# Optimization experiments

Measured on AMD Instinct MI355X. Metric: run time of the kernel, lower is better.

The kernel has to match this reference:

```python
import jax, jax.numpy as jnp
import numpy as np

N_EMBD = 1024
D_K = 1024
D_V = 1024

def setup_inputs() -> dict:
    key = jax.random.key(0)
    k1, k2, k3, k4 = jax.random.split(key, 4)
    B, T = 4, 2048
    std = N_EMBD ** -0.5
    x = jax.random.normal(k1, (B, T, N_EMBD), dtype=jnp.float32)
    Wq = jax.random.normal(k2, (N_EMBD, D_K), dtype=jnp.float32) * std
    Wk = jax.random.normal(k3, (N_EMBD, D_K), dtype=jnp.float32) * std
    Wv = jax.random.normal(k4, (N_EMBD, D_V), dtype=jnp.float32) * std
    return {"x": x, "Wq": Wq, "Wk": Wk, "Wv": Wv}

def reference(x, Wq, Wk, Wv):
    # x: [B, T, C]
    T = x.shape[1]
    q = x @ Wq  # [B, T, d_k]
    k = x @ Wk  # [B, T, d_k]
    v = x @ Wv  # [B, T, d_v]
    scale = Wk.shape[1] ** -0.5
    wei = jnp.einsum('btd,bsd->bts', q, k) * scale  # [B, T, T]
    causal = jnp.tril(jnp.ones((T, T), dtype=bool))
    wei = jnp.where(causal, wei, -jnp.inf)
    wei = jax.nn.softmax(wei, axis=-1)
    return wei @ v  # [B, T, d_v]
```

## Files before the change

kernel.cpp:

```cpp
#include <hip/hip_runtime.h>
#include <hip/hip_bf16.h>
#include <stdint.h>

using bf16_t = __hip_bfloat16;
typedef __bf16 bf16x8 __attribute__((ext_vector_type(8)));
typedef float f32x4 __attribute__((ext_vector_type(4)));

__device__ __forceinline__ void async_lds16(const void* g, void* l) {
  __builtin_amdgcn_global_load_lds(
      (const __attribute__((address_space(1))) void*)g,
      (__attribute__((address_space(3))) void*)l, 16, 0, 0);
}

__device__ __forceinline__ unsigned short f2bf_u16(float f) {
  __hip_bfloat16 h = __float2bfloat16(f);
  return __builtin_bit_cast(unsigned short, h);
}

__device__ __forceinline__ float bf2f(unsigned short u) {
  __hip_bfloat16 h = __builtin_bit_cast(__hip_bfloat16, u);
  return __bfloat162float(h);
}

__global__ __launch_bounds__(256) void convert_all_kernel(
    const float* __restrict__ x, bf16_t* __restrict__ xb,
    const float* __restrict__ Wq, const float* __restrict__ Wk,
    const float* __restrict__ Wv, bf16_t* __restrict__ wt) {
  __shared__ bf16_t tile[32][33];
  const int bid = blockIdx.x;
  if (bid < 8192) {
    size_t i = ((size_t)bid * 256 + threadIdx.x) * 4;
    float4 v = *(const float4*)(x + i);
    ushort4 o;
    o.x = f2bf_u16(v.x);
    o.y = f2bf_u16(v.y);
    o.z = f2bf_u16(v.z);
    o.w = f2bf_u16(v.w);
    *(ushort4*)(xb + i) = o;
    return;
  }
  const int w = bid - 8192;
  const int z = w >> 10;
  const int bxy = w & 1023;
  const float* W = (z == 0) ? Wq : (z == 1) ? Wk : Wv;
  bf16_t* WT = wt + (size_t)z * 1024 * 1024;
  const int tx = threadIdx.x & 31;
  const int ty = threadIdx.x >> 5;
  const int bx = bxy & 31;
  const int by = bxy >> 5;
  const int k0 = by * 32, n0 = bx * 32;
#pragma unroll
  for (int j = 0; j < 32; j += 8)
    tile[ty + j][tx] = __float2bfloat16(W[(size_t)(k0 + ty + j) * 1024 + n0 + tx]);
  __syncthreads();
#pragma unroll
  for (int j = 0; j < 32; j += 8)
    WT[(size_t)(n0 + ty + j) * 1024 + k0 + tx] = tile[tx][ty + j];
}

template <int OUT_MODE, bool CAUSAL_SKIP, bool KLIMIT, bool XCDSWZ>
__global__ __launch_bounds__(512, 2) void gemm_pipe_kernel(
    const bf16_t* __restrict__ A, const bf16_t* __restrict__ BT,
    void* __restrict__ Cv, void* __restrict__ Cv2, void* __restrict__ Cv3,
    int M, int N, int K, int lda, int ldb, int ldc,
    long long aBatch, long long bBatch, long long cBatch) {
  int bx = blockIdx.x, by = blockIdx.y;
  if (XCDSWZ) {
    const int gx = gridDim.x;
    const int nwg = gx * gridDim.y;
    const int id = by * gx + bx;
    const int cpx = nwg >> 3;
    const int swz = (id & 7) * cpx + (id >> 3);
    by = swz / gx;
    bx = swz % gx;
  }
  const int m0 = by * 128;
  const int n0 = bx * 256;
  if (CAUSAL_SKIP && 2 * bx > by) return;
  A += (size_t)blockIdx.z * aBatch;
  BT += (size_t)blockIdx.z * bBatch;
  int nkt = K >> 5;
  if (KLIMIT) {
    int lim = (m0 + 128) >> 5;
    nkt = nkt < lim ? nkt : lim;
  }

  __shared__ bf16_t lsA[3 * 128 * 32];
  __shared__ bf16_t lsB[3 * 256 * 32];

  const int tid = threadIdx.x;
  const int wid = tid >> 6;
  const int lane = tid & 63;
  const int wm = wid >> 2;
  const int wn = wid & 3;

  const int sr = tid >> 2;
  const int ss = tid & 3;
  const int sswz = ss ^ ((sr >> 1) & 3);
  const bf16_t* gA = A + (size_t)(m0 + sr) * lda + sswz * 8;
  const bf16_t* gB0 = BT + (size_t)(n0 + sr) * ldb + sswz * 8;
  const bf16_t* gB1 = BT + (size_t)(n0 + 128 + sr) * ldb + sswz * 8;

  const int kslot = (lane >> 4) ^ ((lane >> 1) & 3);
  const int abase = (wm * 64 + (lane & 15)) * 32 + kslot * 8;
  const int bbase = (wn * 64 + (lane & 15)) * 32 + kslot * 8;

  f32x4 acc[4][4];
  const f32x4 zero = {0.f, 0.f, 0.f, 0.f};
#pragma unroll
  for (int m = 0; m < 4; ++m)
#pragma unroll
    for (int n = 0; n < 4; ++n) acc[m][n] = zero;

  async_lds16(gA, lsA + wid * 512);
  async_lds16(gB0, lsB + wid * 512);
  async_lds16(gB1, lsB + 4096 + wid * 512);
  if (nkt > 1) {
    async_lds16(gA + 32, lsA + 4096 + wid * 512);
    async_lds16(gB0 + 32, lsB + 8192 + wid * 512);
    async_lds16(gB1 + 32, lsB + 8192 + 4096 + wid * 512);
    asm volatile("s_waitcnt vmcnt(3)" ::: "memory");
  } else {
    asm volatile("s_waitcnt vmcnt(0)" ::: "memory");
  }
  __builtin_amdgcn_s_barrier();

  int cb = 0;
  for (int t = 0; t < nkt; ++t) {
    const bf16_t* bufA = lsA + cb * 4096;
    const bf16_t* bufB = lsB + cb * 8192;
    int sb = cb + 2;
    if (sb >= 3) sb -= 3;

    bf16x8 af[4], bfr[4];
#pragma unroll
    for (int mf = 0; mf < 4; ++mf)
      af[mf] = *(const bf16x8*)(bufA + abase + mf * 512);
    bfr[0] = *(const bf16x8*)(bufB + bbase);
    bfr[1] = *(const bf16x8*)(bufB + bbase + 512);
    if (t + 2 < nkt) {
      async_lds16(gA + (t + 2) * 32, lsA + sb * 4096 + wid * 512);
      async_lds16(gB0 + (t + 2) * 32, lsB + sb * 8192 + wid * 512);
    }
    __builtin_amdgcn_s_barrier();
    __builtin_amdgcn_s_setprio(1);
#pragma unroll
    for (int mf = 0; mf < 4; ++mf)
#pragma unroll
      for (int nf = 0; nf < 2; ++nf)
        acc[mf][nf] = __builtin_amdgcn_mfma_f32_16x16x32_bf16(
            af[mf], bfr[nf], acc[mf][nf], 0, 0, 0);
    __builtin_amdgcn_s_setprio(0);
    __builtin_amdgcn_s_barrier();

    bfr[2] = *(const bf16x8*)(bufB + bbase + 1024);
    bfr[3] = *(const bf16x8*)(bufB + bbase + 1536);
    if (t + 2 < nkt)
      async_lds16(gB1 + (t + 2) * 32, lsB + sb * 8192 + 4096 + wid * 512);
    if (t + 2 < nkt) {
      asm volatile("s_waitcnt vmcnt(3)" ::: "memory");
    } else if (t + 2 == nkt) {
      asm volatile("s_waitcnt vmcnt(0)" ::: "memory");
    }
    __builtin_amdgcn_s_barrier();
    __builtin_amdgcn_s_setprio(1);
#pragma unroll
    for (int mf = 0; mf < 4; ++mf)
#pragma unroll
      for (int nf = 2; nf < 4; ++nf)
        acc[mf][nf] = __builtin_amdgcn_mfma_f32_16x16x32_bf16(
            af[mf], bfr[nf], acc[mf][nf], 0, 0, 0);
    __builtin_amdgcn_s_setprio(0);
    __builtin_amdgcn_s_barrier();

    cb = cb + 1;
    if (cb >= 3) cb -= 3;
  }

  const int erow = wm * 64 + (lane >> 4) * 4;
  const int ecol = wn * 64 + (lane & 15);
  if (OUT_MODE == 2) {
    float* C = (float*)Cv + (size_t)blockIdx.z * cBatch;
#pragma unroll
    for (int m = 0; m < 4; ++m)
#pragma unroll
      for (int n = 0; n < 4; ++n)
#pragma unroll
        for (int j = 0; j < 4; ++j) {
          int r = m0 + erow + m * 16 + j;
          int c = n0 + ecol + n * 16;
          C[(size_t)r * ldc + c] = acc[m][n][j];
        }
  } else if (OUT_MODE == 4) {
    bf16_t* C = (bf16_t*)Cv + (size_t)blockIdx.z * cBatch;
#pragma unroll
    for (int m = 0; m < 4; ++m)
#pragma unroll
      for (int n = 0; n < 4; ++n)
#pragma unroll
        for (int j = 0; j < 4; ++j) {
          int r = m0 + erow + m * 16 + j;
          int c = n0 + ecol + n * 16;
          C[(size_t)r * ldc + c] = __float2bfloat16(acc[m][n][j]);
        }
  } else {
    if (n0 < 2048) {
      bf16_t* C = (bf16_t*)((n0 < 1024) ? Cv : Cv2);
      const int cb0 = n0 & 1023;
#pragma unroll
      for (int m = 0; m < 4; ++m)
#pragma unroll
        for (int n = 0; n < 4; ++n)
#pragma unroll
          for (int j = 0; j < 4; ++j) {
            int r = m0 + erow + m * 16 + j;
            int c = cb0 + ecol + n * 16;
            C[(size_t)r * 1024 + c] = __float2bfloat16(acc[m][n][j]);
          }
    } else {
      bf16_t* C = (bf16_t*)Cv3;
      const int d0 = n0 - 2048;
#pragma unroll
      for (int m = 0; m < 4; ++m)
#pragma unroll
        for (int n = 0; n < 4; ++n)
#pragma unroll
          for (int j = 0; j < 4; ++j) {
            int r = m0 + erow + m * 16 + j;
            int d = d0 + ecol + n * 16;
            int b = r >> 11, tt = r & 2047;
            C[((size_t)b * 1024 + d) * 2048 + tt] = __float2bfloat16(acc[m][n][j]);
          }
    }
  }
}

__global__ __launch_bounds__(256) void softmax_causal_kernel(bf16_t* __restrict__ Sb) {
  const int lane = threadIdx.x & 63;
  const int rg = blockIdx.x * 4 + (threadIdx.x >> 6);
  const int b = rg >> 11;
  const int t = rg & 2047;
  bf16_t* srow = Sb + (size_t)b * 8388608 + (size_t)t * 4096;
  const int qmax = t >> 8;

  float v[8][4];
#pragma unroll
  for (int it = 0; it < 8; ++it) {
    if (it <= qmax) {
      ushort4 u = *(const ushort4*)(srow + (it * 64 + lane) * 4);
      v[it][0] = bf2f(u.x);
      v[it][1] = bf2f(u.y);
      v[it][2] = bf2f(u.z);
      v[it][3] = bf2f(u.w);
    } else {
      v[it][0] = v[it][1] = v[it][2] = v[it][3] = 0.f;
    }
  }

  float mx = -3.0e38f;
#pragma unroll
  for (int it = 0; it < 8; ++it) {
    int s0 = (it * 64 + lane) * 4;
    if (s0 + 0 <= t) mx = fmaxf(mx, v[it][0]);
    if (s0 + 1 <= t) mx = fmaxf(mx, v[it][1]);
    if (s0 + 2 <= t) mx = fmaxf(mx, v[it][2]);
    if (s0 + 3 <= t) mx = fmaxf(mx, v[it][3]);
  }
#pragma unroll
  for (int off = 32; off > 0; off >>= 1) mx = fmaxf(mx, __shfl_xor(mx, off, 64));

  const float kMul = 0.03125f * 1.4426950408889634f;
  float p[8][4];
  float sum = 0.f;
#pragma unroll
  for (int it = 0; it < 8; ++it) {
    int s0 = (it * 64 + lane) * 4;
    float e0 = (s0 + 0 <= t) ? exp2f((v[it][0] - mx) * kMul) : 0.f;
    float e1 = (s0 + 1 <= t) ? exp2f((v[it][1] - mx) * kMul) : 0.f;
    float e2 = (s0 + 2 <= t) ? exp2f((v[it][2] - mx) * kMul) : 0.f;
    float e3 = (s0 + 3 <= t) ? exp2f((v[it][3] - mx) * kMul) : 0.f;
    p[it][0] = e0; p[it][1] = e1; p[it][2] = e2; p[it][3] = e3;
    sum += (e0 + e1) + (e2 + e3);
  }
#pragma unroll
  for (int off = 32; off > 0; off >>= 1) sum += __shfl_xor(sum, off, 64);
  const float inv = 1.f / sum;

#pragma unroll
  for (int it = 0; it < 8; ++it) {
    if (it <= qmax) {
      ushort4 o;
      o.x = f2bf_u16(p[it][0] * inv);
      o.y = f2bf_u16(p[it][1] * inv);
      o.z = f2bf_u16(p[it][2] * inv);
      o.w = f2bf_u16(p[it][3] * inv);
      *(ushort4*)(srow + (it * 64 + lane) * 4) = o;
    }
  }
}

extern "C" void kernel_launch(void* const* d_in, const int* in_sizes, int n_in,
                              void* d_out, int out_size, void* d_ws, size_t ws_size,
                              hipStream_t stream) {
  (void)in_sizes; (void)n_in; (void)out_size;
  const float* x = (const float*)d_in[0];
  const float* Wq = (const float*)d_in[1];
  const float* Wk = (const float*)d_in[2];
  const float* Wv = (const float*)d_in[3];
  float* out = (float*)d_out;

  char* ws = (char*)d_ws;
  const size_t NEED = 123731968;
  const bool batched = ws_size >= NEED;

  bf16_t* xb = (bf16_t*)ws;
  bf16_t* Sb;
  bf16_t *WT, *Qb, *Kb, *VT;
  if (batched) {
    Sb = (bf16_t*)ws;
    WT = (bf16_t*)(ws + 67108864);
    Qb = (bf16_t*)(ws + 73400320);
    Kb = (bf16_t*)(ws + 90177536);
    VT = (bf16_t*)(ws + 106954752);
  } else {
    Sb = (bf16_t*)ws;
    WT = (bf16_t*)(ws + 16777216);
    Qb = (bf16_t*)(ws + 16777216 + 6291456);
    Kb = Qb + 8388608;
    VT = Kb + 8388608;
  }

  convert_all_kernel<<<11264, 256, 0, stream>>>(x, xb, Wq, Wk, Wv, WT);

  gemm_pipe_kernel<3, false, false, true><<<dim3(12, 64, 1), 512, 0, stream>>>(
      xb, WT, Qb, Kb, VT, 8192, 3072, 1024, 1024, 1024, 0, 0, 0, 0);

  if (batched) {
    gemm_pipe_kernel<4, true, false, false><<<dim3(8, 16, 4), 512, 0, stream>>>(
        Qb, Kb, Sb, nullptr, nullptr, 2048, 2048, 1024, 1024, 1024, 4096,
        2097152LL, 2097152LL, 8388608LL);
    softmax_causal_kernel<<<2048, 256, 0, stream>>>(Sb);
    gemm_pipe_kernel<2, false, true, false><<<dim3(4, 16, 4), 512, 0, stream>>>(
        Sb, VT, out, nullptr, nullptr, 2048, 1024, 2048, 4096,
        2048, 1024, 8388608LL, 2097152LL, 2097152LL);
  } else {
    for (int b = 0; b < 4; ++b) {
      const size_t qoff = (size_t)b * 2048 * 1024;
      gemm_pipe_kernel<4, true, false, false><<<dim3(8, 16, 1), 512, 0, stream>>>(
          Qb + qoff, Kb + qoff, Sb, nullptr, nullptr, 2048, 2048, 1024, 1024,
          1024, 4096, 0, 0, 0);
      softmax_causal_kernel<<<512, 256, 0, stream>>>(Sb);
      gemm_pipe_kernel<2, false, true, false><<<dim3(4, 16, 1), 512, 0, stream>>>(
          Sb, VT + qoff, out + qoff, nullptr, nullptr, 2048,
          1024, 2048, 4096, 2048, 1024, 0, 0, 0);
    }
  }
}
```

Baseline: 179.9 us.

## Add 256x256-tile GEMM with 64-wide K steps for QKV projection

After: 186.0 us. 3.4% more time.

```diff
diff --git a/kernel.cpp b/kernel.cpp
--- a/kernel.cpp
+++ b/kernel.cpp
@@ -58,12 +58,11 @@
     WT[(size_t)(n0 + ty + j) * 1024 + k0 + tx] = tile[tx][ty + j];
 }
 
-template <int OUT_MODE, bool CAUSAL_SKIP, bool KLIMIT, bool XCDSWZ>
-__global__ __launch_bounds__(512, 2) void gemm_pipe_kernel(
+template <int OUT_MODE, bool XCDSWZ>
+__global__ __launch_bounds__(512, 2) void gemm256_kernel(
     const bf16_t* __restrict__ A, const bf16_t* __restrict__ BT,
     void* __restrict__ Cv, void* __restrict__ Cv2, void* __restrict__ Cv3,
-    int M, int N, int K, int lda, int ldb, int ldc,
-    long long aBatch, long long bBatch, long long cBatch) {
+    int M, int N, int K, int lda, int ldb, int ldc) {
   int bx = blockIdx.x, by = blockIdx.y;
   if (XCDSWZ) {
     const int gx = gridDim.x;
@@ -74,6 +73,182 @@
     by = swz / gx;
     bx = swz % gx;
   }
+  const int m0 = by * 256;
+  const int n0 = bx * 256;
+  const int nkt = K >> 6;
+
+  __shared__ bf16_t lsA[2 * 16384];
+  __shared__ bf16_t lsB[2 * 16384];
+
+  const int tid = threadIdx.x;
+  const int wid = tid >> 6;
+  const int lane = tid & 63;
+  const int wm = wid >> 2;
+  const int wn = wid & 3;
+
+  const int sr = tid >> 2;
+  const int sswz = (tid & 3) ^ ((tid >> 3) & 3);
+  const bf16_t* gA0 = A + (size_t)(m0 + sr) * lda + sswz * 8;
+  const bf16_t* gA1 = A + (size_t)(m0 + 128 + sr) * lda + sswz * 8;
+  const bf16_t* gB0 = BT + (size_t)(n0 + sr) * ldb + sswz * 8;
+  const bf16_t* gB1 = BT + (size_t)(n0 + 128 + sr) * ldb + sswz * 8;
+
+  auto stageA = [&](int t, int kh) {
+    bf16_t* d = lsA + ((t & 1) << 14) + (kh << 13) + (wid << 9);
+    const size_t co = (size_t)(t << 6) + (kh << 5);
+    async_lds16(gA0 + co, d);
+    async_lds16(gA1 + co, d + 4096);
+  };
+  auto stageB = [&](int t, int kh) {
+    bf16_t* d = lsB + ((t & 1) << 14) + (kh << 13) + (wid << 9);
+    const size_t co = (size_t)(t << 6) + (kh << 5);
+    async_lds16(gB0 + co, d);
+    async_lds16(gB1 + co, d + 4096);
+  };
+
+  const int kswz = ((lane >> 4) ^ ((lane >> 1) & 3)) * 8;
+  const int aRd = (wm * 128 + (lane & 15)) * 32 + kswz;
+  const int bRd = (wn * 64 + (lane & 15)) * 32 + kswz;
+
+  f32x4 acc[8][4];
+  const f32x4 zero = {0.f, 0.f, 0.f, 0.f};
+#pragma unroll
+  for (int m = 0; m < 8; ++m)
+#pragma unroll
+    for (int n = 0; n < 4; ++n) acc[m][n] = zero;
+
+  stageA(0, 0);
+  stageB(0, 0);
+  stageA(0, 1);
+  stageB(0, 1);
+  if (nkt > 1) {
+    stageA(1, 0);
+    stageB(1, 0);
+    asm volatile("s_waitcnt vmcnt(4)" ::: "memory");
+  } else {
+    asm volatile("s_waitcnt vmcnt(0)" ::: "memory");
+  }
+  __builtin_amdgcn_s_barrier();
+
+  bf16x8 af[4], bfr[4];
+
+#define PHASE_TAIL()                                      \
+  __builtin_amdgcn_s_barrier();                           \
+  asm volatile("s_waitcnt lgkmcnt(0)" ::: "memory");      \
+  __builtin_amdgcn_s_setprio(1);
+
+#define MFMA16(mh)                                        \
+  _Pragma("unroll") for (int mf = 0; mf < 4; ++mf)        \
+      _Pragma("unroll") for (int nf = 0; nf < 4; ++nf)    \
+          acc[(mh)*4 + mf][nf] = __builtin_amdgcn_mfma_f32_16x16x32_bf16( \
+              af[mf], bfr[nf], acc[(mh)*4 + mf][nf], 0, 0, 0);
+
+  for (int t = 0; t < nkt; ++t) {
+    const bf16_t* bufA = lsA + ((t & 1) << 14);
+    const bf16_t* bufB = lsB + ((t & 1) << 14);
+
+#pragma unroll
+    for (int nf = 0; nf < 4; ++nf)
+      bfr[nf] = *(const bf16x8*)(bufB + (nf << 9) + bRd);
+#pragma unroll
+    for (int mf = 0; mf < 4; ++mf)
+      af[mf] = *(const bf16x8*)(bufA + (mf << 9) + aRd);
+    if (t + 1 < nkt) stageA(t + 1, 1);
+    PHASE_TAIL()
+    MFMA16(0)
+    __builtin_amdgcn_s_setprio(0);
+    __builtin_amdgcn_s_barrier();
+
+#pragma unroll
+    for (int mf = 0; mf < 4; ++mf)
+      af[mf] = *(const bf16x8*)(bufA + ((mf + 4) << 9) + aRd);
+    if (t + 1 < nkt) stageB(t + 1, 1);
+    PHASE_TAIL()
+    MFMA16(1)
+    __builtin_amdgcn_s_setprio(0);
+    __builtin_amdgcn_s_barrier();
+
+#pragma unroll
+    for (int nf = 0; nf < 4; ++nf)
+      bfr[nf] = *(const bf16x8*)(bufB + 8192 + (nf << 9) + bRd);
+#pragma unroll
+    for (int mf = 0; mf < 4; ++mf)
+      af[mf] = *(const bf16x8*)(bufA + 8192 + (mf << 9) + aRd);
+    if (t + 2 < nkt) stageA(t + 2, 0);
+    PHASE_TAIL()
+    MFMA16(0)
+    __builtin_amdgcn_s_setprio(0);
+    __builtin_amdgcn_s_barrier();
+
+#pragma unroll
+    for (int mf = 0; mf < 4; ++mf)
+      af[mf] = *(const bf16x8*)(bufA + 8192 + ((mf + 4) << 9) + aRd);
+    if (t + 2 < nkt) stageB(t + 2, 0);
+    PHASE_TAIL()
+    MFMA16(1)
+    __builtin_amdgcn_s_setprio(0);
+    if (t + 2 < nkt) {
+      asm volatile("s_waitcnt vmcnt(4)" ::: "memory");
+    } else if (t + 1 < nkt) {
+      asm volatile("s_waitcnt vmcnt(0)" ::: "memory");
+    }
+    __builtin_amdgcn_s_barrier();
+  }
+#undef PHASE_TAIL
+#undef MFMA16
+
+  const int erow = wm * 128 + (lane >> 4) * 4;
+  const int ecol = wn * 64 + (lane & 15);
+  if (OUT_MODE == 2) {
+    float* C = (float*)Cv;
+#pragma unroll
+    for (int m = 0; m < 8; ++m)
+#pragma unroll
+      for (int n = 0; n < 4; ++n)
+#pragma unroll
+        for (int j = 0; j < 4; ++j) {
+          int r = m0 + erow + m * 16 + j;
+          int c = n0 + ecol + n * 16;
+          C[(size_t)r * ldc + c] = acc[m][n][j];
+        }
+  } else {
+    if (n0 < 2048) {
+      bf16_t* C = (bf16_t*)((n0 < 1024) ? Cv : Cv2);
+      const int cb0 = n0 & 1023;
+#pragma unroll
+      for (int m = 0; m < 8; ++m)
+#pragma unroll
+        for (int n = 0; n < 4; ++n)
+#pragma unroll
+          for (int j = 0; j < 4; ++j) {
+            int r = m0 + erow + m * 16 + j;
+            int c = cb0 + ecol + n * 16;
+            C[(size_t)r * 1024 + c] = __float2bfloat16(acc[m][n][j]);
+          }
+    } else {
+      bf16_t* C = (bf16_t*)Cv3;
+      const int d0 = n0 - 2048;
+#pragma unroll
+      for (int m = 0; m < 8; ++m)
+#pragma unroll
+        for (int n = 0; n < 4; ++n)
+#pragma unroll
+          for (int j = 0; j < 4; ++j) {
+            int r = m0 + erow + m * 16 + j;
+            int d = d0 + ecol + n * 16;
+            int b = r >> 11, tt = r & 2047;
+            C[((size_t)b * 1024 + d) * 2048 + tt] = __float2bfloat16(acc[m][n][j]);
+          }
+    }
+  }
+}
+
+template <int OUT_MODE, bool CAUSAL_SKIP, bool KLIMIT>
+__global__ __launch_bounds__(512, 2) void gemm_pipe_kernel(
+    const bf16_t* __restrict__ A, const bf16_t* __restrict__ BT,
+    void* __restrict__ Cv, int M, int N, int K, int lda, int ldb, int ldc,
+    long long aBatch, long long bBatch, long long cBatch) {
+  const int bx = blockIdx.x, by = blockIdx.y;
   const int m0 = by * 128;
   const int n0 = bx * 256;
   if (CAUSAL_SKIP && 2 * bx > by) return;
@@ -191,7 +366,7 @@
           int c = n0 + ecol + n * 16;
           C[(size_t)r * ldc + c] = acc[m][n][j];
         }
-  } else if (OUT_MODE == 4) {
+  } else {
     bf16_t* C = (bf16_t*)Cv + (size_t)blockIdx.z * cBatch;
 #pragma unroll
     for (int m = 0; m < 4; ++m)
@@ -203,35 +378,6 @@
           int c = n0 + ecol + n * 16;
           C[(size_t)r * ldc + c] = __float2bfloat16(acc[m][n][j]);
         }
-  } else {
-    if (n0 < 2048) {
-      bf16_t* C = (bf16_t*)((n0 < 1024) ? Cv : Cv2);
-      const int cb0 = n0 & 1023;
-#pragma unroll
-      for (int m = 0; m < 4; ++m)
-#pragma unroll
-        for (int n = 0; n < 4; ++n)
-#pragma unroll
-          for (int j = 0; j < 4; ++j) {
-            int r = m0 + erow + m * 16 + j;
-            int c = cb0 + ecol + n * 16;
-            C[(size_t)r * 1024 + c] = __float2bfloat16(acc[m][n][j]);
-          }
-    } else {
-      bf16_t* C = (bf16_t*)Cv3;
-      const int d0 = n0 - 2048;
-#pragma unroll
-      for (int m = 0; m < 4; ++m)
-#pragma unroll
-        for (int n = 0; n < 4; ++n)
-#pragma unroll
-          for (int j = 0; j < 4; ++j) {
-            int r = m0 + erow + m * 16 + j;
-            int d = d0 + ecol + n * 16;
-            int b = r >> 11, tt = r & 2047;
-            C[((size_t)b * 1024 + d) * 2048 + tt] = __float2bfloat16(acc[m][n][j]);
-          }
-    }
   }
 }
 
@@ -332,27 +478,27 @@
 
   convert_all_kernel<<<11264, 256, 0, stream>>>(x, xb, Wq, Wk, Wv, WT);
 
-  gemm_pipe_kernel<3, false, false, true><<<dim3(12, 64, 1), 512, 0, stream>>>(
-      xb, WT, Qb, Kb, VT, 8192, 3072, 1024, 1024, 1024, 0, 0, 0, 0);
+  gemm256_kernel<3, true><<<dim3(12, 32, 1), 512, 0, stream>>>(
+      xb, WT, Qb, Kb, VT, 8192, 3072, 1024, 1024, 1024, 0);
 
   if (batched) {
-    gemm_pipe_kernel<4, true, false, false><<<dim3(8, 16, 4), 512, 0, stream>>>(
-        Qb, Kb, Sb, nullptr, nullptr, 2048, 2048, 1024, 1024, 1024, 4096,
+    gemm_pipe_kernel<4, true, false><<<dim3(8, 16, 4), 512, 0, stream>>>(
+        Qb, Kb, Sb, 2048, 2048, 1024, 1024, 1024, 4096,
         2097152LL, 2097152LL, 8388608LL);
     softmax_causal_kernel<<<2048, 256, 0, stream>>>(Sb);
-    gemm_pipe_kernel<2, false, true, false><<<dim3(4, 16, 4), 512, 0, stream>>>(
-        Sb, VT, out, nullptr, nullptr, 2048, 1024, 2048, 4096,
-        2048, 1024, 8388608LL, 2097152LL, 2097152LL);
+    gemm_pipe_kernel<2, false, true><<<dim3(4, 16, 4), 512, 0, stream>>>(
+        Sb, VT, out, 2048, 1024, 2048, 4096, 2048, 1024,
+        8388608LL, 2097152LL, 2097152LL);
   } else {
     for (int b = 0; b < 4; ++b) {
       const size_t qoff = (size_t)b * 2048 * 1024;
-      gemm_pipe_kernel<4, true, false, false><<<dim3(8, 16, 1), 512, 0, stream>>>(
-          Qb + qoff, Kb + qoff, Sb, nullptr, nullptr, 2048, 2048, 1024, 1024,
-          1024, 4096, 0, 0, 0);
+      gemm_pipe_kernel<4, true, false><<<dim3(8, 16, 1), 512, 0, stream>>>(
+          Qb + qoff, Kb + qoff, Sb, 2048, 2048, 1024, 1024, 1024, 4096,
+          0, 0, 0);
       softmax_causal_kernel<<<512, 256, 0, stream>>>(Sb);
-      gemm_pipe_kernel<2, false, true, false><<<dim3(4, 16, 1), 512, 0, stream>>>(
-          Sb, VT + qoff, out + qoff, nullptr, nullptr, 2048,
-          1024, 2048, 4096, 2048, 1024, 0, 0, 0);
-    }
-  }
-}
+      gemm_pipe_kernel<2, false, true><<<dim3(4, 16, 1), 512, 0, stream>>>(
+          Sb, VT + qoff, out + qoff, 2048, 1024, 2048, 4096, 2048, 1024,
+          0, 0, 0);
+    }
+  }
+}
```

## Use 128x128 tiles for attention GEMMs with paired causal row balancing

Applied to the files above, without the earlier changes.

Result: faster. 174.8 us (-2.9%).

```diff
diff --git a/kernel.cpp b/kernel.cpp
--- a/kernel.cpp
+++ b/kernel.cpp
@@ -58,14 +58,13 @@
     WT[(size_t)(n0 + ty + j) * 1024 + k0 + tx] = tile[tx][ty + j];
 }
 
-template <int OUT_MODE, bool CAUSAL_SKIP, bool KLIMIT, bool XCDSWZ>
+template <int OUT_MODE>
 __global__ __launch_bounds__(512, 2) void gemm_pipe_kernel(
     const bf16_t* __restrict__ A, const bf16_t* __restrict__ BT,
     void* __restrict__ Cv, void* __restrict__ Cv2, void* __restrict__ Cv3,
-    int M, int N, int K, int lda, int ldb, int ldc,
-    long long aBatch, long long bBatch, long long cBatch) {
+    int M, int N, int K, int lda, int ldb) {
   int bx = blockIdx.x, by = blockIdx.y;
-  if (XCDSWZ) {
+  {
     const int gx = gridDim.x;
     const int nwg = gx * gridDim.y;
     const int id = by * gx + bx;
@@ -76,14 +75,7 @@
   }
   const int m0 = by * 128;
   const int n0 = bx * 256;
-  if (CAUSAL_SKIP && 2 * bx > by) return;
-  A += (size_t)blockIdx.z * aBatch;
-  BT += (size_t)blockIdx.z * bBatch;
-  int nkt = K >> 5;
-  if (KLIMIT) {
-    int lim = (m0 + 128) >> 5;
-    nkt = nkt < lim ? nkt : lim;
-  }
+  const int nkt = K >> 5;
 
   __shared__ bf16_t lsA[3 * 128 * 32];
   __shared__ bf16_t lsB[3 * 256 * 32];
@@ -179,8 +171,9 @@
 
   const int erow = wm * 64 + (lane >> 4) * 4;
   const int ecol = wn * 64 + (lane & 15);
-  if (OUT_MODE == 2) {
-    float* C = (float*)Cv + (size_t)blockIdx.z * cBatch;
+  if (n0 < 2048) {
+    bf16_t* C = (bf16_t*)((n0 < 1024) ? Cv : Cv2);
+    const int cb0 = n0 & 1023;
 #pragma unroll
     for (int m = 0; m < 4; ++m)
 #pragma unroll
@@ -188,11 +181,12 @@
 #pragma unroll
         for (int j = 0; j < 4; ++j) {
           int r = m0 + erow + m * 16 + j;
-          int c = n0 + ecol + n * 16;
-          C[(size_t)r * ldc + c] = acc[m][n][j];
+          int c = cb0 + ecol + n * 16;
+          C[(size_t)r * 1024 + c] = __float2bfloat16(acc[m][n][j]);
         }
-  } else if (OUT_MODE == 4) {
-    bf16_t* C = (bf16_t*)Cv + (size_t)blockIdx.z * cBatch;
+  } else {
+    bf16_t* C = (bf16_t*)Cv3;
+    const int d0 = n0 - 2048;
 #pragma unroll
     for (int m = 0; m < 4; ++m)
 #pragma unroll
@@ -200,36 +194,130 @@
 #pragma unroll
         for (int j = 0; j < 4; ++j) {
           int r = m0 + erow + m * 16 + j;
-          int c = n0 + ecol + n * 16;
-          C[(size_t)r * ldc + c] = __float2bfloat16(acc[m][n][j]);
+          int d = d0 + ecol + n * 16;
+          int b = r >> 11, tt = r & 2047;
+          C[((size_t)b * 1024 + d) * 2048 + tt] = __float2bfloat16(acc[m][n][j]);
         }
-  } else {
-    if (n0 < 2048) {
-      bf16_t* C = (bf16_t*)((n0 < 1024) ? Cv : Cv2);
-      const int cb0 = n0 & 1023;
+  }
+}
+
+template <int OUT_MODE, bool CAUSAL_SKIP, bool PAIRED>
+__global__ __launch_bounds__(512, 2) void gemm128_kernel(
+    const bf16_t* __restrict__ A, const bf16_t* __restrict__ BT,
+    void* __restrict__ Cv, int K, int lda, int ldb, int ldc,
+    long long aBatch, long long bBatch, long long cBatch) {
+  const int bx = blockIdx.x, by = blockIdx.y;
+  if (CAUSAL_SKIP && bx > by) return;
+  const bf16_t* Ab = A + (size_t)blockIdx.z * aBatch;
+  const bf16_t* Bb = BT + (size_t)blockIdx.z * bBatch;
+
+  __shared__ bf16_t lsA[3 * 4096];
+  __shared__ bf16_t lsB[3 * 4096];
+
+  const int tid = threadIdx.x;
+  const int wid = tid >> 6;
+  const int lane = tid & 63;
+  const int wm = wid >> 2;
+  const int wn = wid & 3;
+
+  const int sr = tid >> 2;
+  const int sswz = (tid & 3) ^ ((sr >> 1) & 3);
+  const int n0 = bx * 128;
+  const bf16_t* gB = Bb + (size_t)(n0 + sr) * ldb + sswz * 8;
+
+  const int kslot = (lane >> 4) ^ ((lane >> 1) & 3);
+  const int aRd = (wm * 64 + (lane & 15)) * 32 + kslot * 8;
+  const int bRd = (wn * 32 + (lane & 15)) * 32 + kslot * 8;
+
+  const int njobs = PAIRED ? 2 : 1;
+  for (int job = 0; job < njobs; ++job) {
+    const int byE = (PAIRED && job) ? (15 - by) : by;
+    const int m0 = byE * 128;
+    int nkt = K >> 5;
+    if (PAIRED) {
+      int lim = (m0 + 128) >> 5;
+      nkt = nkt < lim ? nkt : lim;
+    }
+    const bf16_t* gA = Ab + (size_t)(m0 + sr) * lda + sswz * 8;
+
+    f32x4 acc[4][2];
+    const f32x4 zero = {0.f, 0.f, 0.f, 0.f};
+#pragma unroll
+    for (int m = 0; m < 4; ++m)
+#pragma unroll
+      for (int n = 0; n < 2; ++n) acc[m][n] = zero;
+
+    async_lds16(gA, lsA + wid * 512);
+    async_lds16(gB, lsB + wid * 512);
+    if (nkt > 1) {
+      async_lds16(gA + 32, lsA + 4096 + wid * 512);
+      async_lds16(gB + 32, lsB + 4096 + wid * 512);
+      asm volatile("s_waitcnt vmcnt(2)" ::: "memory");
+    } else {
+      asm volatile("s_waitcnt vmcnt(0)" ::: "memory");
+    }
+    __builtin_amdgcn_s_barrier();
+
+    int cb = 0;
+    for (int t = 0; t < nkt; ++t) {
+      const bf16_t* bufA = lsA + cb * 4096;
+      const bf16_t* bufB = lsB + cb * 4096;
+      int sb = cb + 2;
+      if (sb >= 3) sb -= 3;
+
+      bf16x8 af[4], bfr[2];
+#pragma unroll
+      for (int mf = 0; mf < 4; ++mf)
+        af[mf] = *(const bf16x8*)(bufA + aRd + mf * 512);
+      bfr[0] = *(const bf16x8*)(bufB + bRd);
+      bfr[1] = *(const bf16x8*)(bufB + bRd + 512);
+      if (t + 2 < nkt) {
+        async_lds16(gA + (t + 2) * 32, lsA + sb * 4096 + wid * 512);
+        async_lds16(gB + (t + 2) * 32, lsB + sb * 4096 + wid * 512);
+        asm volatile("s_waitcnt vmcnt(2)" ::: "memory");
+      } else if (t + 2 == nkt) {
+        asm volatile("s_waitcnt vmcnt(0)" ::: "memory");
+      }
+      __builtin_amdgcn_s_barrier();
+      __builtin_amdgcn_s_setprio(1);
+#pragma unroll
+      for (int mf = 0; mf < 4; ++mf)
+#pragma unroll
+        for (int nf = 0; nf < 2; ++nf)
+          acc[mf][nf] = __builtin_amdgcn_mfma_f32_16x16x32_bf16(
+              af[mf], bfr[nf], acc[mf][nf], 0, 0, 0);
+      __builtin_amdgcn_s_setprio(0);
+      __builtin_amdgcn_s_barrier();
+
+      cb = cb + 1;
+      if (cb >= 3) cb -= 3;
+    }
+
+    const int erow = wm * 64 + (lane >> 4) * 4;
+    const int ecol = wn * 32 + (lane & 15);
+    if (OUT_MODE == 2) {
+      float* C = (float*)Cv + (size_t)blockIdx.z * cBatch;
 #pragma unroll
       for (int m = 0; m < 4; ++m)
 #pragma unroll
-        for (int n = 0; n < 4; ++n)
+        for (int n = 0; n < 2; ++n)
 #pragma unroll
           for (int j = 0; j < 4; ++j) {
             int r = m0 + erow + m * 16 + j;
-            int c = cb0 + ecol + n * 16;
-            C[(size_t)r * 1024 + c] = __float2bfloat16(acc[m][n][j]);
+            int c = n0 + ecol + n * 16;
+            C[(size_t)r * ldc + c] = acc[m][n][j];
           }
     } else {
-      bf16_t* C = (bf16_t*)Cv3;
-      const int d0 = n0 - 2048;
+      bf16_t* C = (bf16_t*)Cv + (size_t)blockIdx.z * cBatch;
 #pragma unroll
       for (int m = 0; m < 4; ++m)
 #pragma unroll
-        for (int n = 0; n < 4; ++n)
+        for (int n = 0; n < 2; ++n)
 #pragma unroll
           for (int j = 0; j < 4; ++j) {
             int r = m0 + erow + m * 16 + j;
-            int d = d0 + ecol + n * 16;
-            int b = r >> 11, tt = r & 2047;
-            C[((size_t)b * 1024 + d) * 2048 + tt] = __float2bfloat16(acc[m][n][j]);
+            int c = n0 + ecol + n * 16;
+            C[(size_t)r * ldc + c] = __float2bfloat16(acc[m][n][j]);
           }
     }
   }
@@ -332,27 +420,24 @@
 
   convert_all_kernel<<<11264, 256, 0, stream>>>(x, xb, Wq, Wk, Wv, WT);
 
-  gemm_pipe_kernel<3, false, false, true><<<dim3(12, 64, 1), 512, 0, stream>>>(
-      xb, WT, Qb, Kb, VT, 8192, 3072, 1024, 1024, 1024, 0, 0, 0, 0);
-
-  if (batched) {
-    gemm_pipe_kernel<4, true, false, false><<<dim3(8, 16, 4), 512, 0, stream>>>(
-        Qb, Kb, Sb, nullptr, nullptr, 2048, 2048, 1024, 1024, 1024, 4096,
-        2097152LL, 2097152LL, 8388608LL);
-    softmax_causal_kernel<<<2048, 256, 0, stream>>>(Sb);
-    gemm_pipe_kernel<2, false, true, false><<<dim3(4, 16, 4), 512, 0, stream>>>(
-        Sb, VT, out, nullptr, nullptr, 2048, 1024, 2048, 4096,
-        2048, 1024, 8388608LL, 2097152LL, 2097152LL);
-  } else {
-    for (int b = 0; b < 4; ++b) {
-      const size_t qoff = (size_t)b * 2048 * 1024;
-      gemm_pipe_kernel<4, true, false, false><<<dim3(8, 16, 1), 512, 0, stream>>>(
-          Qb + qoff, Kb + qoff, Sb, nullptr, nullptr, 2048, 2048, 1024, 1024,
-          1024, 4096, 0, 0, 0);
-      softmax_causal_kernel<<<512, 256, 0, stream>>>(Sb);
-      gemm_pipe_kernel<2, false, true, false><<<dim3(4, 16, 1), 512, 0, stream>>>(
-          Sb, VT + qoff, out + qoff, nullptr, nullptr, 2048,
-          1024, 2048, 4096, 2048, 1024, 0, 0, 0);
-    }
-  }
-}
+  gemm_pipe_kernel<3><<<dim3(12, 64, 1), 512, 0, stream>>>(
+      xb, WT, Qb, Kb, VT, 8192, 3072, 1024, 1024, 1024);
+
+  const int nbat = batched ? 4 : 1;
+  for (int pass = 0; pass < (batched ? 1 : 4); ++pass) {
+    const size_t qoff = (size_t)pass * 2048 * 1024;
+    const bf16_t* Qp = Qb + qoff;
+    const bf16_t* Kp = Kb + qoff;
+    const bf16_t* Vp = VT + qoff;
+    float* op = out + qoff;
+    gemm128_kernel<5, true, false><<<dim3(16, 16, nbat), 512, 0, stream>>>(
+        Qp, Kp, Sb, 1024, 1024, 1024, 4096,
+        batched ? 2097152LL : 0, batched ? 2097152LL : 0,
+        batched ? 8388608LL : 0);
+    softmax_causal_kernel<<<batched ? 2048 : 512, 256, 0, stream>>>(Sb);
+    gemm128_kernel<2, false, true><<<dim3(8, 8, nbat), 512, 0, stream>>>(
+        Sb, Vp, op, 2048, 4096, 2048, 1024,
+        batched ? 8388608LL : 0, batched ? 2097152LL : 0,
+        batched ? 2097152LL : 0);
+  }
+}
```
